# Performance work log

Hardware: AMD Instinct MI355X
Metric: run time of the kernel (lower is better)

## Reference

```python
import jax, jax.numpy as jnp
import numpy as np

N, H, R, E = 100000, 128, 30, 600000
EPS = 1e-5  # BatchNorm1d default eps


def _rgcn_layer(h, src, dst, etype, W, root, bias):
    """PyG RGCNConv: out = h @ root + bias + sum_r scatter_mean_r(h[src] @ W[r]).
    Mean is per (dst, relation) edge count."""
    n = h.shape[0]
    r_count = W.shape[0]
    seg = dst * r_count + etype                      # combined (dst, rel) segment id
    deg = jax.ops.segment_sum(jnp.ones_like(etype, dtype=h.dtype), seg,
                              num_segments=n * r_count)
    norm = 1.0 / jnp.maximum(deg[seg], 1.0)          # (E,) per-edge mean weight

    def body(out, inp):
        Wr, r = inp
        xr = h @ Wr                                  # (N,H) relation-transformed feats
        contrib = jnp.where((etype == r)[:, None], xr[src] * norm[:, None], 0.0)
        return out + jax.ops.segment_sum(contrib, dst, num_segments=n), None

    out0 = h @ root + bias
    out, _ = jax.lax.scan(body, out0, (W, jnp.arange(r_count)))
    return out


def _bn_relu(h, gamma, beta):
    # BatchNorm1d in training mode: biased batch statistics over the node dim
    mu = h.mean(axis=0)
    var = h.var(axis=0)
    return jax.nn.relu((h - mu) * jax.lax.rsqrt(var + EPS) * gamma + beta)


def setup_inputs() -> dict:
    key = jax.random.key(0)
    ks = jax.random.split(key, 16)
    s = 1.0 / np.sqrt(H)
    return {
        "x": jnp.arange(N, dtype=jnp.int32),
        "edge_index": jax.random.randint(ks[0], (2, E), 0, N, dtype=jnp.int32),
        "edge_type": jax.random.randint(ks[1], (E,), 0, R, dtype=jnp.int32),
        "emb": jax.random.normal(ks[2], (N, H), jnp.float32) * s,
        "W1": jax.random.normal(ks[3], (R, H, H), jnp.float32) * s,
        "root1": jax.random.normal(ks[4], (H, H), jnp.float32) * s,
        "b1": jnp.zeros((H,), jnp.float32),
        "g1": jnp.ones((H,), jnp.float32),
        "be1": jnp.zeros((H,), jnp.float32),
        "W2": jax.random.normal(ks[5], (R, H, H), jnp.float32) * s,
        "root2": jax.random.normal(ks[6], (H, H), jnp.float32) * s,
        "b2": jnp.zeros((H,), jnp.float32),
        "g2": jnp.ones((H,), jnp.float32),
        "be2": jnp.zeros((H,), jnp.float32),
    }


def reference(x, edge_index, edge_type, emb, W1, root1, b1, g1, be1,
              W2, root2, b2, g2, be2):
    src, dst = edge_index[0], edge_index[1]
    h = emb[x]                                        # (N,H) embedding lookup
    h = _bn_relu(_rgcn_layer(h, src, dst, edge_type, W1, root1, b1), g1, be1)
    h = _bn_relu(_rgcn_layer(h, src, dst, edge_type, W2, root2, b2), g2, be2)
    return h  # dropout is identity (deterministic reference)
```

## Files before the change

kernel.cpp:

```cpp
#include <hip/hip_runtime.h>
#include <hip/hip_bf16.h>

#define NN 100000
#define HH 128
#define RR 30
#define RR2 15
#define NE 600000
#define TILE 64
#define EPAD (NE + RR * TILE)
#define NCHMAX (EPAD / TILE)
#define NB_PS ((NN + 255) / 256)
#define NBLK_BN 784
#define RPB_BN 128
#define BN_EPS 1e-5f

typedef __bf16 v8bf __attribute__((ext_vector_type(8)));
typedef float  v4f  __attribute__((ext_vector_type(4)));
typedef unsigned int v4u __attribute__((ext_vector_type(4)));

static __device__ __forceinline__ unsigned short f2b(float f) {
    unsigned int u = __float_as_uint(f);
    unsigned int r = (u + 0x7FFF + ((u >> 16) & 1)) >> 16;
    return (unsigned short)r;
}

static __device__ __forceinline__ unsigned int pk_bf16(float lo, float hi) {
    unsigned int r;
    asm("v_cvt_pk_bf16_f32 %0, %1, %2" : "=v"(r) : "v"(lo), "v"(hi));
    return r;
}

__global__ void k_hist(const int* __restrict__ dst, const int* __restrict__ et,
                       unsigned int* __restrict__ deg16, int* __restrict__ cnt) {
    __shared__ int lh[RR];
    int t = threadIdx.x;
    if (t < RR) lh[t] = 0;
    __syncthreads();
    int i = blockIdx.x * blockDim.x + t;
    if (i < NE) {
        int d = dst[i], r = et[i];
        atomicAdd(&deg16[(size_t)d * RR2 + (r >> 1)], 1u << ((r & 1) * 16));
        atomicAdd(&lh[r], 1);
    }
    __syncthreads();
    if (t < RR && lh[t]) atomicAdd(&cnt[t], lh[t]);
}

__global__ void k_degsum(const unsigned int* __restrict__ deg16,
                         int* __restrict__ cnt_d) {
    int d = blockIdx.x * blockDim.x + threadIdx.x;
    if (d >= NN) return;
    int s = 0;
#pragma unroll
    for (int r2 = 0; r2 < RR2; ++r2) {
        unsigned int v = deg16[(size_t)d * RR2 + r2];
        s += (int)(v & 0xffffu) + (int)(v >> 16);
    }
    cnt_d[d] = s;
}

__global__ void k_scan(const int* __restrict__ cnt, int* __restrict__ cursor,
                       int* __restrict__ totals,
                       int* __restrict__ src_s, int* __restrict__ dst_s,
                       float* __restrict__ norm_s, int* __restrict__ dpos_s,
                       int* __restrict__ chunk_rel, int need_dst) {
    __shared__ int off[RR + 1];
    if (threadIdx.x == 0) {
        int acc = 0;
        for (int r = 0; r < RR; ++r) {
            off[r] = acc;
            acc += (cnt[r] + TILE - 1) / TILE;
        }
        off[RR] = acc;
        totals[0] = acc * TILE;
    }
    __syncthreads();
    for (int r = 0; r < RR; ++r) {
        for (int c = off[r] + (int)threadIdx.x; c < off[r + 1]; c += blockDim.x)
            chunk_rel[c] = r;
        int begin = off[r] * TILE + cnt[r];
        int end   = off[r + 1] * TILE;
        for (int p = begin + (int)threadIdx.x; p < end; p += blockDim.x) {
            src_s[p] = 0; norm_s[p] = 0.f;
            dpos_s[p] = NE;
            if (need_dst) dst_s[p] = 0;
        }
    }
    if (threadIdx.x == 0)
        for (int r = 0; r < RR; ++r) cursor[r] = off[r] * TILE;
}

__global__ void k_psum1(const int* __restrict__ c, int* __restrict__ bsum) {
    __shared__ int sh[256];
    int i = blockIdx.x * 256 + threadIdx.x;
    sh[threadIdx.x] = (i < NN) ? c[i] : 0;
    __syncthreads();
    for (int s = 128; s > 0; s >>= 1) {
        if (threadIdx.x < s) sh[threadIdx.x] += sh[threadIdx.x + s];
        __syncthreads();
    }
    if (threadIdx.x == 0) bsum[blockIdx.x] = sh[0];
}

__global__ void k_psum2(int* __restrict__ bsum) {
    __shared__ int sh[512];
    int t = threadIdx.x;
    sh[t] = (t < NB_PS) ? bsum[t] : 0;
    __syncthreads();
    if (t == 0) {
        int acc = 0;
        for (int b = 0; b < NB_PS; ++b) { int v = sh[b]; sh[b] = acc; acc += v; }
    }
    __syncthreads();
    if (t < NB_PS) bsum[t] = sh[t];
}

__global__ void k_psum3(const int* __restrict__ c, const int* __restrict__ bscan,
                        int* __restrict__ off, int* __restrict__ cur) {
    __shared__ int sh[256];
    int t = threadIdx.x;
    int i = blockIdx.x * 256 + t;
    int v = (i < NN) ? c[i] : 0;
    sh[t] = v;
    __syncthreads();
    for (int s = 1; s < 256; s <<= 1) {
        int a = (t >= s) ? sh[t - s] : 0;
        __syncthreads();
        sh[t] += a;
        __syncthreads();
    }
    int excl = sh[t] - v + bscan[blockIdx.x];
    if (i < NN) { off[i] = excl; cur[i] = excl; }
    if (i == 0) off[NN] = NE;
}

__global__ void k_scatter(const int* __restrict__ src, const int* __restrict__ dst,
                          const int* __restrict__ et,
                          const unsigned int* __restrict__ deg16,
                          int* __restrict__ cursor, int* __restrict__ cursor_dst,
                          int* __restrict__ src_s, int* __restrict__ dst_s,
                          float* __restrict__ norm_s, int* __restrict__ dpos_s,
                          int need_dst) {
    __shared__ int lh[RR];
    __shared__ int lbase[RR];
    int t = threadIdx.x;
    if (t < RR) lh[t] = 0;
    __syncthreads();
    int i = blockIdx.x * blockDim.x + t;
    int r = 0, d = 0, lrank = 0;
    bool valid = (i < NE);
    if (valid) {
        r = et[i]; d = dst[i];
        lrank = atomicAdd(&lh[r], 1);
    }
    __syncthreads();
    if (t < RR && lh[t]) lbase[t] = atomicAdd(&cursor[t], lh[t]);
    __syncthreads();
    if (valid) {
        int pos = lbase[r] + lrank;
        src_s[pos] = src[i];
        if (need_dst) dst_s[pos] = d;
        int dg = (int)((deg16[(size_t)d * RR2 + (r >> 1)] >> ((r & 1) * 16)) & 0xffffu);
        norm_s[pos] = 1.0f / (float)(dg > 1 ? dg : 1);
        dpos_s[pos] = atomicAdd(&cursor_dst[d], 1);
    }
}

__global__ void k_convW(const float* __restrict__ W, unsigned short* __restrict__ Wt,
                        int total) {
    int idx = blockIdx.x * blockDim.x + threadIdx.x;
    if (idx >= total) return;
    int m = idx / (HH * HH);
    int rem = idx % (HH * HH);
    int k = rem / HH, c = rem % HH;
    Wt[m * HH * HH + c * HH + k] = f2b(W[idx]);
}

__global__ void k_embed(const int* __restrict__ x, const float* __restrict__ emb,
                        unsigned int* __restrict__ hb2) {
    int idx = blockIdx.x * blockDim.x + threadIdx.x;
    if (idx >= NN * HH / 2) return;
    int i = idx >> 6;
    int j2 = (idx & 63) * 2;
    const float* p = emb + (size_t)x[i] * HH + j2;
    hb2[idx] = pk_bf16(p[0], p[1]);
}

__global__ __launch_bounds__(256) void k_rootagg(const unsigned short* __restrict__ hb,
                                                 const unsigned short* __restrict__ rootT,
                                                 const float* __restrict__ bias,
                                                 const int* __restrict__ off,
                                                 const unsigned short* __restrict__ xe,
                                                 float* __restrict__ tmp) {
    __shared__ __align__(16) unsigned short Ws[64][HH + 8];
    int t = threadIdx.x;
    int base = blockIdx.x * TILE;

    int w = t >> 6, lane = t & 63;
    int lr16 = lane & 15, kg = lane >> 4;
    int slot = w * 16 + lr16;
    int drow = base + slot;
    bool valid = (drow < NN);
    int dsafe = valid ? drow : 0;

    v8bf xf[4];
    const unsigned short* hrow = hb + (size_t)dsafe * HH + kg * 8;
#pragma unroll
    for (int kk = 0; kk < 4; ++kk)
        xf[kk] = *reinterpret_cast<const v8bf*>(hrow + kk * 32);

    v4f acc[8];
#pragma unroll
    for (int n = 0; n < 8; ++n) acc[n] = (v4f){0.f, 0.f, 0.f, 0.f};

    for (int i = 0; i < 4; ++i) {
        int idx = t + 256 * i;
        int row = idx >> 4, g = idx & 15;
        *reinterpret_cast<uint4*>(&Ws[row][g * 8]) =
            *reinterpret_cast<const uint4*>(rootT + row * HH + g * 8);
    }
    __syncthreads();
#pragma unroll
    for (int n = 0; n < 4; ++n)
#pragma unroll
        for (int kk = 0; kk < 4; ++kk) {
            v8bf wf = *reinterpret_cast<const v8bf*>(&Ws[n * 16 + lr16][kk * 32 + kg * 8]);
            acc[n] = __builtin_amdgcn_mfma_f32_16x16x32_bf16(wf, xf[kk], acc[n], 0, 0, 0);
        }
    __syncthreads();
    for (int i = 0; i < 4; ++i) {
        int idx = t + 256 * i;
        int row = idx >> 4, g = idx & 15;
        *reinterpret_cast<uint4*>(&Ws[row][g * 8]) =
            *reinterpret_cast<const uint4*>(rootT + (64 + row) * HH + g * 8);
    }
    __syncthreads();
#pragma unroll
    for (int n = 4; n < 8; ++n)
#pragma unroll
        for (int kk = 0; kk < 4; ++kk) {
            v8bf wf = *reinterpret_cast<const v8bf*>(&Ws[(n - 4) * 16 + lr16][kk * 32 + kg * 8]);
            acc[n] = __builtin_amdgcn_mfma_f32_16x16x32_bf16(wf, xf[kk], acc[n], 0, 0, 0);
        }

    int s = valid ? off[drow] : 0;
    int e = valid ? off[drow + 1] : 0;
    int p = s;
    for (; p + 1 < e; p += 2) {
        const unsigned short* xr0 = xe + (size_t)p * HH + kg * 4;
        const unsigned short* xr1 = xr0 + HH;
        uint2 u0[8], u1[8];
#pragma unroll
        for (int n = 0; n < 8; ++n) {
            u0[n] = *reinterpret_cast<const uint2*>(xr0 + n * 16);
            u1[n] = *reinterpret_cast<const uint2*>(xr1 + n * 16);
        }
#pragma unroll
        for (int n = 0; n < 8; ++n) {
            acc[n][0] += __uint_as_float(u0[n].x << 16) + __uint_as_float(u1[n].x << 16);
            acc[n][1] += __uint_as_float(u0[n].x & 0xffff0000u) + __uint_as_float(u1[n].x & 0xffff0000u);
            acc[n][2] += __uint_as_float(u0[n].y << 16) + __uint_as_float(u1[n].y << 16);
            acc[n][3] += __uint_as_float(u0[n].y & 0xffff0000u) + __uint_as_float(u1[n].y & 0xffff0000u);
        }
    }
    if (p < e) {
        const unsigned short* xr = xe + (size_t)p * HH + kg * 4;
#pragma unroll
        for (int n = 0; n < 8; ++n) {
            uint2 u = *reinterpret_cast<const uint2*>(xr + n * 16);
            acc[n][0] += __uint_as_float(u.x << 16);
            acc[n][1] += __uint_as_float(u.x & 0xffff0000u);
            acc[n][2] += __uint_as_float(u.y << 16);
            acc[n][3] += __uint_as_float(u.y & 0xffff0000u);
        }
    }

    if (valid) {
        float* orow = tmp + (size_t)drow * HH + kg * 4;
#pragma unroll
        for (int n = 0; n < 8; ++n) {
            v4f b = *reinterpret_cast<const v4f*>(bias + n * 16 + kg * 4);
            *reinterpret_cast<v4f*>(orow + n * 16) = acc[n] + b;
        }
    }
}

__global__ __launch_bounds__(256) void k_rootgemm(const unsigned short* __restrict__ hb,
                                                  const unsigned short* __restrict__ rootT,
                                                  const float* __restrict__ bias,
                                                  float* __restrict__ tmp) {
    __shared__ __align__(16) unsigned short Xs[TILE][HH + 8];
    __shared__ __align__(16) unsigned short Ws[HH][HH + 8];
    int base = blockIdx.x * TILE;
    int t = threadIdx.x;

    {
        int l = t >> 2, lr = t & 3;
        int row = base + l;
        for (int i = 0; i < 4; ++i) {
            int g = lr + 4 * i;
            uint4 v = {0u, 0u, 0u, 0u};
            if (row < NN) v = *reinterpret_cast<const uint4*>(hb + (size_t)row * HH + g * 8);
            *reinterpret_cast<uint4*>(&Xs[l][g * 8]) = v;
        }
    }
    for (int i = 0; i < 8; ++i) {
        int idx = t + 256 * i;
        int row = idx >> 4, g = idx & 15;
        *reinterpret_cast<uint4*>(&Ws[row][g * 8]) =
            *reinterpret_cast<const uint4*>(rootT + row * HH + g * 8);
    }
    __syncthreads();

    int w = t >> 6, lane = t & 63;
    int lr16 = lane & 15, kg = lane >> 4;
    v4f acc[8];
    for (int n = 0; n < 8; ++n) acc[n] = (v4f){0.f, 0.f, 0.f, 0.f};
#pragma unroll
    for (int kk = 0; kk < 4; ++kk) {
        int k0 = kk * 32 + kg * 8;
        v8bf a = *reinterpret_cast<const v8bf*>(&Xs[w * 16 + lr16][k0]);
#pragma unroll
        for (int n = 0; n < 8; ++n) {
            v8bf b = *reinterpret_cast<const v8bf*>(&Ws[n * 16 + lr16][k0]);
            acc[n] = __builtin_amdgcn_mfma_f32_16x16x32_bf16(a, b, acc[n], 0, 0, 0);
        }
    }
#pragma unroll
    for (int n = 0; n < 8; ++n)
        for (int j = 0; j < 4; ++j) {
            int row = base + w * 16 + kg * 4 + j;
            int col = n * 16 + lr16;
            if (row < NN) tmp[(size_t)row * HH + col] = acc[n][j] + bias[col];
        }
}

__global__ __launch_bounds__(256) void k_edgegemm_x(const unsigned short* __restrict__ hb,
                                                    const unsigned short* __restrict__ Wt,
                                                    const int* __restrict__ src_s,
                                                    const int* __restrict__ chunk_rel,
                                                    const float* __restrict__ norm_s,
                                                    const int* __restrict__ dpos_s,
                                                    const int* __restrict__ totals,
                                                    unsigned short* __restrict__ xe) {
    int ebase = blockIdx.x * TILE;
    if (ebase >= totals[0]) return;
    __shared__ __align__(16) unsigned short S[HH * (HH + 8)];
    int t = threadIdx.x;
    int rel = chunk_rel[blockIdx.x];

    const unsigned short* Wr = Wt + (size_t)rel * HH * HH;
    for (int i = 0; i < 8; ++i) {
        int idx = t + 256 * i;
        int row = idx >> 4, g = idx & 15;
        *reinterpret_cast<uint4*>(&S[row * (HH + 8) + g * 8]) =
            *reinterpret_cast<const uint4*>(Wr + row * HH + g * 8);
    }

    int w = t >> 6, lane = t & 63;
    int lr16 = lane & 15, kg = lane >> 4;
    int slot = w * 16 + lr16;
    int srow = src_s[ebase + slot];
    float nrm = norm_s[ebase + slot];

    v8bf xf[4];
    const unsigned short* hrow = hb + (size_t)srow * HH + kg * 8;
#pragma unroll
    for (int kk = 0; kk < 4; ++kk)
        xf[kk] = *reinterpret_cast<const v8bf*>(hrow + kk * 32);

    __syncthreads();

    v4f acc[8];
#pragma unroll
    for (int n = 0; n < 8; ++n) acc[n] = (v4f){0.f, 0.f, 0.f, 0.f};
#pragma unroll
    for (int n = 0; n < 8; ++n)
#pragma unroll
        for (int kk = 0; kk < 4; ++kk) {
            v8bf wf = *reinterpret_cast<const v8bf*>(
                &S[(n * 16 + lr16) * (HH + 8) + kk * 32 + kg * 8]);
            acc[n] = __builtin_amdgcn_mfma_f32_16x16x32_bf16(wf, xf[kk], acc[n], 0, 0, 0);
        }

    __syncthreads();

    int c = slot & 7;
#pragma unroll
    for (int n = 0; n < 8; ++n) {
        unsigned int w0 = pk_bf16(acc[n][0] * nrm, acc[n][1] * nrm);
        unsigned int w1 = pk_bf16(acc[n][2] * nrm, acc[n][3] * nrm);
        unsigned long long p = (unsigned long long)w0 | ((unsigned long long)w1 << 32);
        int a = n * 4 + kg;
        int sw = (((a >> 1) ^ c) << 1) | (a & 1);
        *reinterpret_cast<unsigned long long*>(&S[slot * HH + sw * 4]) = p;
    }
    __syncthreads();
    {
        int l = t >> 2, lr = t & 3;
        size_t drow = (size_t)dpos_s[ebase + l];
        int cs = l & 7;
        unsigned short* orow = xe + drow * HH;
#pragma unroll
        for (int i = 0; i < 4; ++i) {
            int j = lr + 4 * i;
            v4u v = *reinterpret_cast<const v4u*>(&S[l * HH + (j ^ cs) * 8]);
            *reinterpret_cast<v4u*>(orow + j * 8) = v;
        }
    }
}

__global__ __launch_bounds__(256) void k_edgegemm_at(const unsigned short* __restrict__ hb,
                                                     const unsigned short* __restrict__ Wt,
                                                     const int* __restrict__ src_s,
                                                     const int* __restrict__ dst_s,
                                                     const int* __restrict__ chunk_rel,
                                                     const float* __restrict__ norm_s,
                                                     const int* __restrict__ totals,
                                                     float* __restrict__ tmp) {
    int ebase = blockIdx.x * TILE;
    if (ebase >= totals[0]) return;
    __shared__ __align__(16) unsigned short Xs[TILE][HH + 8];
    __shared__ __align__(16) unsigned short Ws[HH][HH + 8];
    __shared__ int   src_l[TILE];
    __shared__ int   dst_l[TILE];
    __shared__ float nrm_l[TILE];
    int t = threadIdx.x;
    if (t < TILE) {
        src_l[t] = src_s[ebase + t];
        dst_l[t] = dst_s[ebase + t];
        nrm_l[t] = norm_s[ebase + t];
    }
    int rel = chunk_rel[blockIdx.x];
    __syncthreads();
    {
        int l = t >> 2, lr = t & 3;
        int srow = src_l[l];
        for (int i = 0; i < 4; ++i) {
            int g = lr + 4 * i;
            *reinterpret_cast<uint4*>(&Xs[l][g * 8]) =
                *reinterpret_cast<const uint4*>(hb + (size_t)srow * HH + g * 8);
        }
    }
    const unsigned short* Wr = Wt + (size_t)rel * HH * HH;
    for (int i = 0; i < 8; ++i) {
        int idx = t + 256 * i;
        int row = idx >> 4, g = idx & 15;
        *reinterpret_cast<uint4*>(&Ws[row][g * 8]) =
            *reinterpret_cast<const uint4*>(Wr + row * HH + g * 8);
    }
    __syncthreads();
    int w = t >> 6, lane = t & 63;
    int lr16 = lane & 15, kg = lane >> 4;
    v4f acc[8];
    for (int n = 0; n < 8; ++n) acc[n] = (v4f){0.f, 0.f, 0.f, 0.f};
#pragma unroll
    for (int kk = 0; kk < 4; ++kk) {
        int k0 = kk * 32 + kg * 8;
        v8bf a = *reinterpret_cast<const v8bf*>(&Xs[w * 16 + lr16][k0]);
#pragma unroll
        for (int n = 0; n < 8; ++n) {
            v8bf b = *reinterpret_cast<const v8bf*>(&Ws[n * 16 + lr16][k0]);
            acc[n] = __builtin_amdgcn_mfma_f32_16x16x32_bf16(a, b, acc[n], 0, 0, 0);
        }
    }
#pragma unroll
    for (int n = 0; n < 8; ++n)
        for (int j = 0; j < 4; ++j) {
            int slot = w * 16 + kg * 4 + j;
            int col  = n * 16 + lr16;
            atomicAdd(&tmp[(size_t)dst_l[slot] * HH + col], acc[n][j] * nrm_l[slot]);
        }
}

__global__ __launch_bounds__(256) void k_bnsum1(const float* __restrict__ tmp,
                                                float* __restrict__ psum,
                                                float* __restrict__ psq) {
    int t = threadIdx.x;
    int rg = t >> 5, lane = t & 31;
    int base = blockIdx.x * RPB_BN;
    v4f s = {0.f, 0.f, 0.f, 0.f}, q = {0.f, 0.f, 0.f, 0.f};
#pragma unroll 4
    for (int i = 0; i < RPB_BN / 8; ++i) {
        int row = base + rg + 8 * i;
        if (row < NN) {
            v4f v = *reinterpret_cast<const v4f*>(tmp + (size_t)row * HH + lane * 4);
            s += v; q += v * v;
        }
    }
    __shared__ v4f shs[8][32], shq[8][32];
    shs[rg][lane] = s; shq[rg][lane] = q;
    __syncthreads();
    if (rg == 0) {
        v4f ts = shs[0][lane], tq = shq[0][lane];
#pragma unroll
        for (int k = 1; k < 8; ++k) { ts += shs[k][lane]; tq += shq[k][lane]; }
        int b = blockIdx.x;
#pragma unroll
        for (int j = 0; j < 4; ++j) {
            psum[(size_t)(lane * 4 + j) * NBLK_BN + b] = ts[j];
            psq [(size_t)(lane * 4 + j) * NBLK_BN + b] = tq[j];
        }
    }
}

__global__ void k_bnsum2(const float* __restrict__ psum, const float* __restrict__ psq,
                         const float* __restrict__ g, const float* __restrict__ be,
                         float* __restrict__ sc_g, float* __restrict__ shf_g) {
    __shared__ float ssum[HH], ssq[HH];
    int t = threadIdx.x;
    int col = t & 127;
    const float* row = ((t < 128) ? psum : psq) + (size_t)col * NBLK_BN;
    v4f a = {0.f, 0.f, 0.f, 0.f};
    for (int i = 0; i < NBLK_BN / 4; ++i)
        a += *reinterpret_cast<const v4f*>(row + i * 4);
    float acc = a[0] + a[1] + a[2] + a[3];
    if (t < 128) ssum[col] = acc; else ssq[col] = acc;
    __syncthreads();
    if (t < 128) {
        float inv_n = 1.0f / (float)NN;
        float mean = ssum[col] * inv_n;
        float var = ssq[col] * inv_n - mean * mean;
        float sc = g[col] * rsqrtf(var + BN_EPS);
        sc_g[col] = sc;
        shf_g[col] = be[col] - mean * sc;
    }
}

__global__ void k_bnapply(const float* __restrict__ tmp, const float* __restrict__ sc_g,
                          const float* __restrict__ shf_g,
                          unsigned short* __restrict__ hout,
                          float* __restrict__ fout, int write_bf16) {
    int idx = blockIdx.x * blockDim.x + threadIdx.x;
    if (idx >= NN * HH / 4) return;
    int c4 = (idx & 31) * 4;
    v4f v  = *reinterpret_cast<const v4f*>(tmp + (size_t)idx * 4);
    v4f sc = *reinterpret_cast<const v4f*>(sc_g + c4);
    v4f sh = *reinterpret_cast<const v4f*>(shf_g + c4);
    v4f r;
#pragma unroll
    for (int j = 0; j < 4; ++j) r[j] = fmaxf(v[j] * sc[j] + sh[j], 0.f);
    if (write_bf16) {
        uint2 u;
        u.x = pk_bf16(r[0], r[1]);
        u.y = pk_bf16(r[2], r[3]);
        *reinterpret_cast<uint2*>(hout + (size_t)idx * 4) = u;
    } else {
        *reinterpret_cast<v4f*>(fout + (size_t)idx * 4) = r;
    }
}

constexpr size_t OFF_DEG  = 0;
constexpr size_t OFF_HB   = OFF_DEG + (size_t)NN * RR2 * 4;
constexpr size_t OFF_TMP  = OFF_HB + (size_t)NN * HH * 2;
constexpr size_t OFF_W1T  = OFF_TMP + (size_t)NN * HH * 4;
constexpr size_t OFF_W2T  = OFF_W1T + (size_t)RR * HH * HH * 2;
constexpr size_t OFF_R1T  = OFF_W2T + (size_t)RR * HH * HH * 2;
constexpr size_t OFF_R2T  = OFF_R1T + (size_t)HH * HH * 2;
constexpr size_t OFF_SRCS = OFF_R2T + (size_t)HH * HH * 2;
constexpr size_t OFF_DSTS = OFF_SRCS + (size_t)EPAD * 4;
constexpr size_t OFF_NRMS = OFF_DSTS + (size_t)EPAD * 4;
constexpr size_t OFF_DPOS = OFF_NRMS + (size_t)EPAD * 4;
constexpr size_t OFF_CREL = OFF_DPOS + (size_t)EPAD * 4;
constexpr size_t OFF_CNTD = OFF_CREL + ((size_t)NCHMAX * 4 + 255 & ~(size_t)255);
constexpr size_t OFF_OFFD = OFF_CNTD + ((size_t)(NN + 1) * 4 + 255 & ~(size_t)255);
constexpr size_t OFF_CURD = OFF_OFFD + ((size_t)(NN + 1) * 4 + 255 & ~(size_t)255);
constexpr size_t OFF_BSUM = OFF_CURD + ((size_t)NN * 4 + 255 & ~(size_t)255);
constexpr size_t OFF_CTRL = OFF_BSUM + ((size_t)NB_PS * 4 + 255 & ~(size_t)255);
constexpr size_t OFF_SC   = OFF_CTRL + 512;
constexpr size_t OFF_SHF  = OFF_SC + 512;
constexpr size_t OFF_PSUM = OFF_SHF + 512;
constexpr size_t OFF_PSQ  = OFF_PSUM + (size_t)HH * NBLK_BN * 4;
constexpr size_t OFF_XE   = (OFF_PSQ + (size_t)HH * NBLK_BN * 4 + 255) & ~(size_t)255;
constexpr size_t WS_MIN   = OFF_XE;
constexpr size_t WS_FULL  = OFF_XE + (size_t)EPAD * HH * 2;

extern "C" void kernel_launch(void* const* d_in, const int* in_sizes, int n_in,
                              void* d_out, int out_size, void* d_ws, size_t ws_size,
                              hipStream_t stream) {
    const int*   x     = (const int*)d_in[0];
    const int*   eidx  = (const int*)d_in[1];
    const int*   et    = (const int*)d_in[2];
    const float* emb   = (const float*)d_in[3];
    const float* W1    = (const float*)d_in[4];
    const float* root1 = (const float*)d_in[5];
    const float* b1    = (const float*)d_in[6];
    const float* g1    = (const float*)d_in[7];
    const float* be1   = (const float*)d_in[8];
    const float* W2    = (const float*)d_in[9];
    const float* root2 = (const float*)d_in[10];
    const float* b2    = (const float*)d_in[11];
    const float* g2    = (const float*)d_in[12];
    const float* be2   = (const float*)d_in[13];
    float* out = (float*)d_out;

    if (ws_size < WS_MIN) return;
    const bool full = (ws_size >= WS_FULL);
    const int need_dst = full ? 0 : 1;

    char* ws = (char*)d_ws;
    unsigned int* deg16 = (unsigned int*)(ws + OFF_DEG);
    unsigned short* hb = (unsigned short*)(ws + OFF_HB);
    float* tmp    = (float*)(ws + OFF_TMP);
    unsigned short* W1t = (unsigned short*)(ws + OFF_W1T);
    unsigned short* W2t = (unsigned short*)(ws + OFF_W2T);
    unsigned short* r1t = (unsigned short*)(ws + OFF_R1T);
    unsigned short* r2t = (unsigned short*)(ws + OFF_R2T);
    int*   src_s  = (int*)(ws + OFF_SRCS);
    int*   dst_s  = (int*)(ws + OFF_DSTS);
    float* norm_s = (float*)(ws + OFF_NRMS);
    int*   dpos_s = (int*)(ws + OFF_DPOS);
    int*   crel   = (int*)(ws + OFF_CREL);
    int*   cnt_d  = (int*)(ws + OFF_CNTD);
    int*   off_d  = (int*)(ws + OFF_OFFD);
    int*   cur_d  = (int*)(ws + OFF_CURD);
    int*   bsum   = (int*)(ws + OFF_BSUM);
    int*   cnt    = (int*)(ws + OFF_CTRL);
    int*   cursor = cnt + 32;
    int*   totals = cnt + 64;
    float* sc_g   = (float*)(ws + OFF_SC);
    float* shf_g  = (float*)(ws + OFF_SHF);
    float* psum   = (float*)(ws + OFF_PSUM);
    float* psq    = (float*)(ws + OFF_PSQ);
    unsigned short* xe = (unsigned short*)(ws + OFF_XE);

    const int* srcp = eidx;
    const int* dstp = eidx + NE;

    hipMemsetAsync(deg16, 0, (size_t)NN * RR2 * 4, stream);
    hipMemsetAsync(cnt, 0, 512, stream);

    k_hist<<<(NE + 255) / 256, 256, 0, stream>>>(dstp, et, deg16, cnt);
    k_degsum<<<(NN + 255) / 256, 256, 0, stream>>>(deg16, cnt_d);
    k_scan<<<1, 256, 0, stream>>>(cnt, cursor, totals, src_s, dst_s, norm_s,
                                  dpos_s, crel, need_dst);
    k_psum1<<<NB_PS, 256, 0, stream>>>(cnt_d, bsum);
    k_psum2<<<1, 512, 0, stream>>>(bsum);
    k_psum3<<<NB_PS, 256, 0, stream>>>(cnt_d, bsum, off_d, cur_d);
    k_scatter<<<(NE + 255) / 256, 256, 0, stream>>>(srcp, dstp, et, deg16, cursor, cur_d,
                                                    src_s, dst_s, norm_s, dpos_s,
                                                    need_dst);
    k_convW<<<(RR * HH * HH + 255) / 256, 256, 0, stream>>>(W1, W1t, RR * HH * HH);
    k_convW<<<(RR * HH * HH + 255) / 256, 256, 0, stream>>>(W2, W2t, RR * HH * HH);
    k_convW<<<(HH * HH + 255) / 256, 256, 0, stream>>>(root1, r1t, HH * HH);
    k_convW<<<(HH * HH + 255) / 256, 256, 0, stream>>>(root2, r2t, HH * HH);
    k_embed<<<(NN * HH / 2 + 255) / 256, 256, 0, stream>>>(x, emb, (unsigned int*)hb);

    const unsigned short* Wts[2] = {W1t, W2t};
    const unsigned short* rts[2] = {r1t, r2t};
    const float* biases[2] = {b1, b2};
    const float* gs[2]     = {g1, g2};
    const float* bes[2]    = {be1, be2};

    for (int layer = 0; layer < 2; ++layer) {
        if (full) {
            k_edgegemm_x<<<EPAD / TILE, 256, 0, stream>>>(hb, Wts[layer], src_s, crel,
                                                          norm_s, dpos_s, totals, xe);
            k_rootagg<<<(NN + TILE - 1) / TILE, 256, 0, stream>>>(hb, rts[layer],
                                                                  biases[layer], off_d,
                                                                  xe, tmp);
        } else {
            k_rootgemm<<<(NN + TILE - 1) / TILE, 256, 0, stream>>>(hb, rts[layer],
                                                                   biases[layer], tmp);
            k_edgegemm_at<<<EPAD / TILE, 256, 0, stream>>>(hb, Wts[layer], src_s, dst_s,
                                                           crel, norm_s, totals, tmp);
        }
        k_bnsum1<<<NBLK_BN, 256, 0, stream>>>(tmp, psum, psq);
        k_bnsum2<<<1, 256, 0, stream>>>(psum, psq, gs[layer], bes[layer], sc_g, shf_g);
        k_bnapply<<<(NN * HH / 4 + 255) / 256, 256, 0, stream>>>(tmp, sc_g, shf_g,
                                                                 hb, out, layer == 0);
    }
}
```

Before: 480.1 us.

## Sort destination nodes by in-degree to balance rootagg aggregation work

Adds a counting sort of destination nodes by in-degree, using a histogram, a prefix scan and a scatter into a permutation array. k_rootagg then processes nodes in permuted order, so nodes with similar edge counts land in the same wavefront and block. The aim is to cut divergence and load imbalance in the per-node aggregation loop. The cost is three small preprocessing kernels, an extra indirection, and scattered rather than sequential row access to hb and tmp.

```diff
diff --git a/kernel.cpp b/kernel.cpp
--- a/kernel.cpp
+++ b/kernel.cpp
@@ -12,6 +12,7 @@
 #define NB_PS ((NN + 255) / 256)
 #define NBLK_BN 784
 #define RPB_BN 128
+#define DBKT 512
 #define BN_EPS 1e-5f
 
 typedef __bf16 v8bf __attribute__((ext_vector_type(8)));
@@ -134,6 +135,54 @@
     if (i == 0) off[NN] = NE;
 }
 
+__global__ void k_dhist(const int* __restrict__ cnt_d, int* __restrict__ dhist) {
+    __shared__ int lh[DBKT];
+    for (int i = threadIdx.x; i < DBKT; i += 256) lh[i] = 0;
+    __syncthreads();
+    int d = blockIdx.x * 256 + threadIdx.x;
+    if (d < NN) {
+        int b = cnt_d[d]; b = b < DBKT - 1 ? b : DBKT - 1;
+        atomicAdd(&lh[b], 1);
+    }
+    __syncthreads();
+    for (int i = threadIdx.x; i < DBKT; i += 256)
+        if (lh[i]) atomicAdd(&dhist[i], lh[i]);
+}
+
+__global__ void k_dprefix(const int* __restrict__ dhist, int* __restrict__ dcur) {
+    __shared__ int sh[DBKT];
+    int t = threadIdx.x;
+    int v = dhist[t];
+    sh[t] = v;
+    __syncthreads();
+    for (int s = 1; s < DBKT; s <<= 1) {
+        int a = (t >= s) ? sh[t - s] : 0;
+        __syncthreads();
+        sh[t] += a;
+        __syncthreads();
+    }
+    dcur[t] = sh[t] - v;
+}
+
+__global__ void k_dscatter(const int* __restrict__ cnt_d, int* __restrict__ dcur,
+                           int* __restrict__ perm) {
+    __shared__ int lh[DBKT], lbase[DBKT];
+    for (int i = threadIdx.x; i < DBKT; i += 256) lh[i] = 0;
+    __syncthreads();
+    int d = blockIdx.x * 256 + threadIdx.x;
+    int b = 0, lrank = 0;
+    bool valid = (d < NN);
+    if (valid) {
+        b = cnt_d[d]; b = b < DBKT - 1 ? b : DBKT - 1;
+        lrank = atomicAdd(&lh[b], 1);
+    }
+    __syncthreads();
+    for (int i = threadIdx.x; i < DBKT; i += 256)
+        if (lh[i]) lbase[i] = atomicAdd(&dcur[i], lh[i]);
+    __syncthreads();
+    if (valid) perm[lbase[b] + lrank] = d;
+}
+
 __global__ void k_scatter(const int* __restrict__ src, const int* __restrict__ dst,
                           const int* __restrict__ et,
                           const unsigned int* __restrict__ deg16,
@@ -190,6 +239,7 @@
                                                  const unsigned short* __restrict__ rootT,
                                                  const float* __restrict__ bias,
                                                  const int* __restrict__ off,
+                                                 const int* __restrict__ perm,
                                                  const unsigned short* __restrict__ xe,
                                                  float* __restrict__ tmp) {
     __shared__ __align__(16) unsigned short Ws[64][HH + 8];
@@ -199,12 +249,12 @@
     int w = t >> 6, lane = t & 63;
     int lr16 = lane & 15, kg = lane >> 4;
     int slot = w * 16 + lr16;
-    int drow = base + slot;
-    bool valid = (drow < NN);
-    int dsafe = valid ? drow : 0;
+    int pidx = base + slot;
+    bool valid = (pidx < NN);
+    int drow = valid ? perm[pidx] : 0;
 
     v8bf xf[4];
-    const unsigned short* hrow = hb + (size_t)dsafe * HH + kg * 8;
+    const unsigned short* hrow = hb + (size_t)drow * HH + kg * 8;
 #pragma unroll
     for (int kk = 0; kk < 4; ++kk)
         xf[kk] = *reinterpret_cast<const v8bf*>(hrow + kk * 32);
@@ -565,7 +615,10 @@
 constexpr size_t OFF_CNTD = OFF_CREL + ((size_t)NCHMAX * 4 + 255 & ~(size_t)255);
 constexpr size_t OFF_OFFD = OFF_CNTD + ((size_t)(NN + 1) * 4 + 255 & ~(size_t)255);
 constexpr size_t OFF_CURD = OFF_OFFD + ((size_t)(NN + 1) * 4 + 255 & ~(size_t)255);
-constexpr size_t OFF_BSUM = OFF_CURD + ((size_t)NN * 4 + 255 & ~(size_t)255);
+constexpr size_t OFF_PERM = OFF_CURD + ((size_t)NN * 4 + 255 & ~(size_t)255);
+constexpr size_t OFF_DH   = OFF_PERM + ((size_t)NN * 4 + 255 & ~(size_t)255);
+constexpr size_t OFF_DC   = OFF_DH + DBKT * 4;
+constexpr size_t OFF_BSUM = OFF_DC + DBKT * 4;
 constexpr size_t OFF_CTRL = OFF_BSUM + ((size_t)NB_PS * 4 + 255 & ~(size_t)255);
 constexpr size_t OFF_SC   = OFF_CTRL + 512;
 constexpr size_t OFF_SHF  = OFF_SC + 512;
@@ -614,6 +667,9 @@
     int*   cnt_d  = (int*)(ws + OFF_CNTD);
     int*   off_d  = (int*)(ws + OFF_OFFD);
     int*   cur_d  = (int*)(ws + OFF_CURD);
+    int*   perm   = (int*)(ws + OFF_PERM);
+    int*   dhist  = (int*)(ws + OFF_DH);
+    int*   dcur   = (int*)(ws + OFF_DC);
     int*   bsum   = (int*)(ws + OFF_BSUM);
     int*   cnt    = (int*)(ws + OFF_CTRL);
     int*   cursor = cnt + 32;
@@ -629,6 +685,7 @@
 
     hipMemsetAsync(deg16, 0, (size_t)NN * RR2 * 4, stream);
     hipMemsetAsync(cnt, 0, 512, stream);
+    hipMemsetAsync(dhist, 0, DBKT * 4, stream);
 
     k_hist<<<(NE + 255) / 256, 256, 0, stream>>>(dstp, et, deg16, cnt);
     k_degsum<<<(NN + 255) / 256, 256, 0, stream>>>(deg16, cnt_d);
@@ -637,6 +694,9 @@
     k_psum1<<<NB_PS, 256, 0, stream>>>(cnt_d, bsum);
     k_psum2<<<1, 512, 0, stream>>>(bsum);
     k_psum3<<<NB_PS, 256, 0, stream>>>(cnt_d, bsum, off_d, cur_d);
+    k_dhist<<<(NN + 255) / 256, 256, 0, stream>>>(cnt_d, dhist);
+    k_dprefix<<<1, DBKT, 0, stream>>>(dhist, dcur);
+    k_dscatter<<<(NN + 255) / 256, 256, 0, stream>>>(cnt_d, dcur, perm);
     k_scatter<<<(NE + 255) / 256, 256, 0, stream>>>(srcp, dstp, et, deg16, cursor, cur_d,
                                                     src_s, dst_s, norm_s, dpos_s,
                                                     need_dst);
@@ -658,7 +718,7 @@
                                                           norm_s, dpos_s, totals, xe);
             k_rootagg<<<(NN + TILE - 1) / TILE, 256, 0, stream>>>(hb, rts[layer],
                                                                   biases[layer], off_d,
-                                                                  xe, tmp);
+                                                                  perm, xe, tmp);
         } else {
             k_rootgemm<<<(NN + TILE - 1) / TILE, 256, 0, stream>>>(hb, rts[layer],
                                                                    biases[layer], tmp);
```

New measurement: 506.1 us. 5.4% more time.
